# Performance work log

Measured on AMD Instinct MI355X. Metric: run time of the kernel, lower is better.

The kernel has to match this reference:

```python
import jax, jax.numpy as jnp
import numpy as np

B, F, SF = 2, 5, 15          # batch, query frames, num_shots*sframe
C, KD, VD = 1024, 128, 512   # encoder_dim, keydim, valdim
H = W = 32                   # l3 feature map (output stride 8 on 256x256)


def _conv(x, w, b, pad):
    y = jax.lax.conv_general_dilated(
        x, w, window_strides=(1, 1), padding=[(pad, pad), (pad, pad)],
        dimension_numbers=("NCHW", "OIHW", "NCHW"))
    return y + b[None, :, None, None]


def setup_inputs() -> dict:
    key = jax.random.key(0)
    ks = jax.random.split(key, 8)
    s = 0.02
    return {
        "query_feat": jax.random.normal(ks[0], (B * F, C, H, W), jnp.float32),
        "support_fg_feat": jax.random.normal(ks[1], (B * SF, C, H, W), jnp.float32),
        "w_sk": jax.random.normal(ks[2], (KD, C, 3, 3), jnp.float32) * s,
        "b_sk": jnp.zeros((KD,), jnp.float32),
        "w_sv": jax.random.normal(ks[3], (VD, C, 3, 3), jnp.float32) * s,
        "b_sv": jnp.zeros((VD,), jnp.float32),
        "w_qq": jax.random.normal(ks[4], (KD, C, 3, 3), jnp.float32) * s,
        "b_qq": jnp.zeros((KD,), jnp.float32),
        "w_qk": jax.random.normal(ks[5], (KD, C, 3, 3), jnp.float32) * s,
        "b_qk": jnp.zeros((KD,), jnp.float32),
        "w_cq": jax.random.normal(ks[6], (VD, C, 1, 1), jnp.float32) * s,
        "b_cq": jnp.zeros((VD,), jnp.float32),
    }


def reference(query_feat, support_fg_feat, w_sk, b_sk, w_sv, b_sv,
              w_qq, b_qq, w_qk, b_qk, w_cq, b_cq):
    hw = H * W
    # QKV projections (3x3 convs)
    sk = _conv(support_fg_feat, w_sk, b_sk, 1)   # [B*SF, KD, H, W]
    sv = _conv(support_fg_feat, w_sv, b_sv, 1)   # [B*SF, VD, H, W]
    qq = _conv(query_feat, w_qq, b_qq, 1)        # [B*F, KD, H, W]
    qk = _conv(query_feat, w_qk, b_qk, 1)        # [B*F, KD, H, W]

    # support K: [B, SF*hw, KD];  support V: [B, VD, SF*hw]
    support_k = sk.reshape(B, SF, KD, H, W).transpose(0, 2, 1, 3, 4)
    support_k = support_k.reshape(B, KD, SF * hw).transpose(0, 2, 1)
    support_v = sv.reshape(B, SF, VD, H, W).transpose(0, 2, 1, 3, 4)
    support_v = support_v.reshape(B, VD, SF * hw)

    qq5 = qq.reshape(B, F, KD, H, W)
    qk5 = qk.reshape(B, F, KD, H, W)
    mid = F // 2
    scale = 1.0 / jnp.sqrt(jnp.float32(KD))

    # stage 1: middle-frame query attends into support memory
    middle_q = qq5[:, mid].reshape(B, KD, hw)                 # [B, KD, hw]
    P1 = jnp.einsum("bkc,bcq->bkq", support_k, middle_q) * scale  # [B, SF*hw, hw]
    P1 = jax.nn.softmax(P1, axis=1)
    new_V = jnp.einsum("bvk,bkq->bvq", support_v, P1)          # [B, VD, hw]

    # stage 2: all-frame queries attend into middle-frame keys
    middle_K = qk5[:, mid].reshape(B, KD, hw).transpose(0, 2, 1)   # [B, hw, KD]
    qq_flat = qq5.transpose(0, 2, 1, 3, 4).reshape(B, KD, F * hw)  # [B, KD, F*hw]
    P2 = jnp.einsum("bkc,bcq->bkq", middle_K, qq_flat) * scale     # [B, hw, F*hw]
    P2 = jax.nn.softmax(P2, axis=1)
    Out = jnp.einsum("bvk,bkq->bvq", new_V, P2)                    # [B, VD, F*hw]

    after = Out.reshape(B, VD, F, H, W).transpose(0, 2, 1, 3, 4)
    after = after.reshape(B * F, VD, H, W)
    qf = _conv(query_feat, w_cq, b_cq, 0)                          # [B*F, VD, H, W]
    return jnp.concatenate([after, qf], axis=1)                    # [B*F, 2*VD, H, W]
```

## Files before the change

kernel.cpp:

```cpp
#include <hip/hip_runtime.h>
#include <cstdint>

typedef unsigned short u16;
typedef __attribute__((ext_vector_type(8))) u16 u16x8;
typedef __attribute__((ext_vector_type(4))) u16 u16x4;
typedef __attribute__((ext_vector_type(8))) _Float16 f16x8;
typedef __attribute__((ext_vector_type(4))) float f32x4;

__device__ __forceinline__ u16 f2h(float f) {
  _Float16 h = (_Float16)f;
  return __builtin_bit_cast(u16, h);
}
__device__ __forceinline__ float h2f(u16 b) {
  _Float16 h = __builtin_bit_cast(_Float16, b);
  return (float)h;
}
__device__ __forceinline__ void gll16(const void* g, void* l) {
  auto gp = reinterpret_cast<const __attribute__((address_space(1))) unsigned int*>(
      reinterpret_cast<uintptr_t>(g));
  auto lp = reinterpret_cast<__attribute__((address_space(3))) unsigned int*>(
      reinterpret_cast<uintptr_t>(l));
  __builtin_amdgcn_global_load_lds(gp, lp, 16, 0, 0);
}

__global__ __launch_bounds__(256) void pad_nhwc(const float* __restrict__ in,
                                                u16* __restrict__ outp) {
  const int img = blockIdx.x >> 5;
  const int y   = blockIdx.x & 31;
  __shared__ float tile[32][33];
  const int tid = threadIdx.x;
  u16* base = outp + (long)img * 34 * 34 * 1024;
  const u16x8 z8 = {0, 0, 0, 0, 0, 0, 0, 0};
  {
    u16* r = base + (long)(y + 1) * 34 * 1024;
    if (tid < 128) *(u16x8*)&r[tid * 8] = z8;
    else *(u16x8*)&r[33 * 1024 + (tid - 128) * 8] = z8;
  }
  if (y == 0) {
    for (int i = tid * 8; i < 34816; i += 2048) *(u16x8*)&base[i] = z8;
  }
  if (y == 31) {
    u16* r = base + 33L * 34 * 1024;
    for (int i = tid * 8; i < 34816; i += 2048) *(u16x8*)&r[i] = z8;
  }
  const int xi = tid & 31, ci = tid >> 5;
  const int xo = tid >> 3, q = tid & 7;
  const float* ip = in + (long)img * 1048576 + y * 32;
  u16* op = base + ((long)(y + 1) * 34 + 1) * 1024;
  for (int c0 = 0; c0 < 1024; c0 += 32) {
#pragma unroll
    for (int k2 = 0; k2 < 4; k2++)
      tile[k2 * 8 + ci][xi] = ip[(long)(c0 + k2 * 8 + ci) * 1024 + xi];
    __syncthreads();
    u16x4 o4;
#pragma unroll
    for (int r = 0; r < 4; r++) o4[r] = f2h(tile[q * 4 + r][xo]);
    *(u16x4*)&op[(long)xo * 1024 + c0 + q * 4] = o4;
    __syncthreads();
  }
}

__device__ __forceinline__ void wre3_body(const float* __restrict__ wp,
                                          u16* __restrict__ op, float* buf) {
  for (int i = threadIdx.x; i < 9216; i += 256) buf[i] = wp[i];
  __syncthreads();
  for (int k = threadIdx.x; k < 9216; k += 256) {
    int t = k >> 10, c = k & 1023;
    op[k] = f2h(buf[c * 9 + t]);
  }
}
__global__ __launch_bounds__(256) void wprep(
    const float* __restrict__ w_sk, const float* __restrict__ w_sv,
    const float* __restrict__ w_qq, const float* __restrict__ w_qk,
    const float* __restrict__ w_cq, u16* __restrict__ WTSK,
    u16* __restrict__ WTSV, u16* __restrict__ WTQQK, u16* __restrict__ WCQ) {
  __shared__ float buf[9216];
  const int b = blockIdx.x;
  if (b < 128) {
    wre3_body(w_sk + (long)b * 9216, WTSK + (long)b * 9216, buf);
  } else if (b < 640) {
    const int oc = b - 128;
    wre3_body(w_sv + (long)oc * 9216, WTSV + (long)oc * 9216, buf);
  } else if (b < 768) {
    const int oc = b - 640;
    wre3_body(w_qq + (long)oc * 9216, WTQQK + (long)oc * 9216, buf);
  } else if (b < 896) {
    const int oc = b - 768;
    wre3_body(w_qk + (long)oc * 9216, WTQQK + (long)(oc + 128) * 9216, buf);
  } else {
    const int i = (b - 896) * 1024 + threadIdx.x * 4;
#pragma unroll
    for (int r = 0; r < 4; r++) WCQ[i + r] = f2h(w_cq[i + r]);
  }
}

__global__ __launch_bounds__(256) void row_softmax60(u16* __restrict__ P) {
  u16* p = P + (long)blockIdx.x * 15360;
  const int tid = threadIdx.x;
  __shared__ float rm[4], rs[4];
  u16x4 v[15];
#pragma unroll
  for (int j = 0; j < 15; j++)
    v[j] = *(const u16x4*)(p + ((tid + (j << 8)) << 2));
  float m = -3.0e38f;
#pragma unroll
  for (int j = 0; j < 15; j++)
#pragma unroll
    for (int e = 0; e < 4; e++) m = fmaxf(m, h2f(v[j][e]));
#pragma unroll
  for (int o = 32; o > 0; o >>= 1) m = fmaxf(m, __shfl_xor(m, o, 64));
  if ((tid & 63) == 0) rm[tid >> 6] = m;
  __syncthreads();
  const float M = fmaxf(fmaxf(rm[0], rm[1]), fmaxf(rm[2], rm[3]));
  float s = 0.f;
#pragma unroll
  for (int j = 0; j < 15; j++)
#pragma unroll
    for (int e = 0; e < 4; e++) s += __expf(h2f(v[j][e]) - M);
#pragma unroll
  for (int o = 32; o > 0; o >>= 1) s += __shfl_xor(s, o, 64);
  if ((tid & 63) == 0) rs[tid >> 6] = s;
  __syncthreads();
  const float inv = 1.0f / (rs[0] + rs[1] + rs[2] + rs[3]);
#pragma unroll
  for (int j = 0; j < 15; j++) {
    u16x4 o4;
#pragma unroll
    for (int e = 0; e < 4; e++) o4[e] = f2h(__expf(h2f(v[j][e]) - M) * inv);
    *(u16x4*)(p + ((tid + (j << 8)) << 2)) = o4;
  }
}

__global__ __launch_bounds__(256) void row_softmax4(u16* __restrict__ P) {
  u16* p = P + (long)blockIdx.x * 1024;
  const int tid = threadIdx.x;
  __shared__ float rm[4], rs[4];
  u16x4 v = *(const u16x4*)(p + (tid << 2));
  float m = fmaxf(fmaxf(h2f(v[0]), h2f(v[1])), fmaxf(h2f(v[2]), h2f(v[3])));
#pragma unroll
  for (int o = 32; o > 0; o >>= 1) m = fmaxf(m, __shfl_xor(m, o, 64));
  if ((tid & 63) == 0) rm[tid >> 6] = m;
  __syncthreads();
  const float M = fmaxf(fmaxf(rm[0], rm[1]), fmaxf(rm[2], rm[3]));
  float s = 0.f;
#pragma unroll
  for (int e = 0; e < 4; e++) s += __expf(h2f(v[e]) - M);
#pragma unroll
  for (int o = 32; o > 0; o >>= 1) s += __shfl_xor(s, o, 64);
  if ((tid & 63) == 0) rs[tid >> 6] = s;
  __syncthreads();
  const float inv = 1.0f / (rs[0] + rs[1] + rs[2] + rs[3]);
  u16x4 o4;
#pragma unroll
  for (int e = 0; e < 4; e++) o4[e] = f2h(__expf(h2f(v[e]) - M) * inv);
  *(u16x4*)(p + (tid << 2)) = o4;
}

__global__ __launch_bounds__(256) void reduce4(const float* __restrict__ part,
                                               u16* __restrict__ o) {
  long j = ((long)blockIdx.x * 256 + threadIdx.x) * 4;
  int b = (int)(j >> 19);
  long i = j & 524287;
  const float* p = part + (long)b * 2097152 + i;
  f32x4 s = *(const f32x4*)&p[0];
#pragma unroll
  for (int c = 1; c < 4; c++) s = s + *(const f32x4*)&p[(long)c * 524288];
  u16x4 o4;
#pragma unroll
  for (int r = 0; r < 4; r++) o4[r] = f2h(s[r]);
  *(u16x4*)&o[j] = o4;
}
__global__ __launch_bounds__(256) void reduce_sk(const float* __restrict__ part,
                                                 const float* __restrict__ bias,
                                                 u16* __restrict__ o) {
  long i = ((long)blockIdx.x * 256 + threadIdx.x) * 4;
  f32x4 s = *(const f32x4*)&part[i];
  s = s + *(const f32x4*)&part[i + 3932160];
  f32x4 bb = *(const f32x4*)&bias[(int)(i & 127)];
  u16x4 o4;
#pragma unroll
  for (int r = 0; r < 4; r++) o4[r] = f2h(s[r] + bb[r]);
  *(u16x4*)&o[i] = o4;
}
__global__ __launch_bounds__(256) void reduce_qqk(
    const float* __restrict__ part, const float* __restrict__ b_qq,
    const float* __restrict__ b_qk, u16* __restrict__ QQR,
    u16* __restrict__ QKR) {
  long i = ((long)blockIdx.x * 256 + threadIdx.x) * 4;
  const int n = (int)(i >> 8), m = (int)(i & 255);
  f32x4 s = *(const f32x4*)&part[i];
  s = s + *(const f32x4*)&part[i + 2621440];
  const int lo = (m < 128);
  const int mm = m & 127;
  const float* bs = lo ? b_qq : b_qk;
  f32x4 bb = *(const f32x4*)&bs[mm];
  u16* dst = (lo ? QQR : QKR) + (long)n * 128 + mm;
  u16x4 o4;
#pragma unroll
  for (int r = 0; r < 4; r++) o4[r] = f2h(s[r] + bb[r]);
  *(u16x4*)dst = o4;
}

__global__ __launch_bounds__(512, 1)
void gemm256(const u16* __restrict__ A, const u16* __restrict__ B,
             const float* __restrict__ bias, u16* __restrict__ out) {
  __shared__ u16 lds[65536];
  const int tid = threadIdx.x, lane = tid & 63, wave = tid >> 6;
  const int nwg = gridDim.x * gridDim.y;
  int wg = blockIdx.x + gridDim.x * blockIdx.y;
  wg = (wg & 7) * (nwg >> 3) + (wg >> 3);
  const int ntile = wg % gridDim.x;
  const int mtile = wg / gridDim.x;

  const int slog = (lane & 7) ^ ((lane >> 3) & 7);
  const u16* aS[4];
  const u16* bS[4];
  int aD[4], bD[4];
#pragma unroll
  for (int j = 0; j < 4; j++) {
    const int r = wave * 32 + j * 8 + (lane >> 3);
    aS[j] = A + (long)(mtile * 256 + r) * 9216 + slog * 8;
    aD[j] = (wave * 32 + j * 8) * 64;
    const int n = ntile * 256 + r;
    const int img = n >> 10, p = n & 1023;
    const int y = p >> 5, x = p & 31;
    bS[j] = B + ((long)((img * 34 + y) * 34 + x)) * 1024 + slog * 8;
    bD[j] = 16384 + (wave * 32 + j * 8) * 64;
  }

  const int g = lane >> 4, l15 = lane & 15;
  const int wm = wave >> 2, wn = wave & 3;
  int aRow[8], bRow[4], sx[2];
#pragma unroll
  for (int mi = 0; mi < 8; mi++) aRow[mi] = (wm * 128 + mi * 16 + l15) * 64;
#pragma unroll
  for (int ni = 0; ni < 4; ni++) bRow[ni] = 16384 + (wn * 64 + ni * 16 + l15) * 64;
#pragma unroll
  for (int ks = 0; ks < 2; ks++) sx[ks] = ((ks * 4 + g) ^ (l15 & 7)) * 8;

  f32x4 acc[8][4];
  const f32x4 zero = {0.f, 0.f, 0.f, 0.f};
#pragma unroll
  for (int i = 0; i < 8; i++)
#pragma unroll
    for (int j = 0; j < 4; j++) acc[i][j] = zero;

  const int nkt = 144;
  {
#pragma unroll
    for (int j = 0; j < 4; j++) gll16(aS[j], &lds[aD[j]]);
#pragma unroll
    for (int j = 0; j < 4; j++) gll16(bS[j], &lds[bD[j]]);
    asm volatile("s_waitcnt vmcnt(0)" ::: "memory");
    __builtin_amdgcn_s_barrier();
  }

  for (int kt = 0; kt < nkt; ++kt) {
    const int buf = (kt & 1) << 15;
    const int nbuf = buf ^ 32768;
    const bool st = (kt + 1 < nkt);
    const int kb1 = (kt + 1) << 6;
    int bAdd = 0;
    if (st) {
      const int t = kb1 >> 10, c0 = kb1 & 1023;
      const int dy = t / 3, dx = t - dy * 3;
      bAdd = (dy * 34 + dx) * 1024 + c0;
    }
    f16x8 afr[4], bfr[4];
#pragma unroll
    for (int mi = 0; mi < 4; mi++) afr[mi] = *(const f16x8*)&lds[buf + aRow[mi] + sx[0]];
#pragma unroll
    for (int ni = 0; ni < 4; ni++) bfr[ni] = *(const f16x8*)&lds[buf + bRow[ni] + sx[0]];
    if (st) {
      gll16(aS[0] + kb1, &lds[nbuf + aD[0]]);
      gll16(aS[1] + kb1, &lds[nbuf + aD[1]]);
      gll16(bS[0] + bAdd, &lds[nbuf + bD[0]]);
      gll16(bS[1] + bAdd, &lds[nbuf + bD[1]]);
    }
    __builtin_amdgcn_s_barrier();
    __builtin_amdgcn_s_setprio(1);
#pragma unroll
    for (int mi = 0; mi < 4; mi++)
#pragma unroll
      for (int ni = 0; ni < 4; ni++)
        acc[mi][ni] = __builtin_amdgcn_mfma_f32_16x16x32_f16(afr[mi], bfr[ni], acc[mi][ni], 0, 0, 0);
    __builtin_amdgcn_s_setprio(0);
    __builtin_amdgcn_s_barrier();
#pragma unroll
    for (int mi = 0; mi < 4; mi++) afr[mi] = *(const f16x8*)&lds[buf + aRow[mi + 4] + sx[0]];
    if (st) {
      gll16(aS[2] + kb1, &lds[nbuf + aD[2]]);
      gll16(aS[3] + kb1, &lds[nbuf + aD[3]]);
      gll16(bS[2] + bAdd, &lds[nbuf + bD[2]]);
      gll16(bS[3] + bAdd, &lds[nbuf + bD[3]]);
    }
    __builtin_amdgcn_s_barrier();
    __builtin_amdgcn_s_setprio(1);
#pragma unroll
    for (int mi = 0; mi < 4; mi++)
#pragma unroll
      for (int ni = 0; ni < 4; ni++)
        acc[mi + 4][ni] = __builtin_amdgcn_mfma_f32_16x16x32_f16(afr[mi], bfr[ni], acc[mi + 4][ni], 0, 0, 0);
    __builtin_amdgcn_s_setprio(0);
    __builtin_amdgcn_s_barrier();
#pragma unroll
    for (int mi = 0; mi < 4; mi++) afr[mi] = *(const f16x8*)&lds[buf + aRow[mi] + sx[1]];
#pragma unroll
    for (int ni = 0; ni < 4; ni++) bfr[ni] = *(const f16x8*)&lds[buf + bRow[ni] + sx[1]];
    __builtin_amdgcn_s_barrier();
    __builtin_amdgcn_s_setprio(1);
#pragma unroll
    for (int mi = 0; mi < 4; mi++)
#pragma unroll
      for (int ni = 0; ni < 4; ni++)
        acc[mi][ni] = __builtin_amdgcn_mfma_f32_16x16x32_f16(afr[mi], bfr[ni], acc[mi][ni], 0, 0, 0);
    __builtin_amdgcn_s_setprio(0);
    __builtin_amdgcn_s_barrier();
#pragma unroll
    for (int mi = 0; mi < 4; mi++) afr[mi] = *(const f16x8*)&lds[buf + aRow[mi + 4] + sx[1]];
    __builtin_amdgcn_s_barrier();
    __builtin_amdgcn_s_setprio(1);
#pragma unroll
    for (int mi = 0; mi < 4; mi++)
#pragma unroll
      for (int ni = 0; ni < 4; ni++)
        acc[mi + 4][ni] = __builtin_amdgcn_mfma_f32_16x16x32_f16(afr[mi], bfr[ni], acc[mi + 4][ni], 0, 0, 0);
    __builtin_amdgcn_s_setprio(0);
    asm volatile("s_waitcnt vmcnt(0)" ::: "memory");
    __builtin_amdgcn_s_barrier();
  }

  const int b0 = 0;
  (void)b0;
#pragma unroll
  for (int mi = 0; mi < 8; mi++) {
#pragma unroll
    for (int ni = 0; ni < 4; ni++) {
      f32x4 v = acc[mi][ni];
      const int m0 = mtile * 256 + wm * 128 + mi * 16 + g * 4;
      const int n = ntile * 256 + wn * 64 + ni * 16 + l15;
      const int b = (n >= 15360) ? 1 : 0;
      const int rem = n - b * 15360;
#pragma unroll
      for (int r = 0; r < 4; r++) {
        const int m = m0 + r;
        out[(long)b * 7864320 + (long)m * 15360 + rem] = f2h(v[r] + bias[m]);
      }
    }
  }
}

template <int BMODE, int EPI, int SPLITK>
__global__ __launch_bounds__(256, 2)
void gemm_nt(const u16* __restrict__ A, long Azoff, int Astride,
             const u16* __restrict__ B, long Bzoff, int Bstride,
             int K, float scale,
             const float* __restrict__ bias, const float* __restrict__ bias2,
             void* __restrict__ out0, void* __restrict__ out1,
             long out_zoff, int ldo) {
  __shared__ u16 lds[4 * 8192];
  const int tid = threadIdx.x;
  const int lane = tid & 63;
  const int wave = tid >> 6;
  const int mtile = blockIdx.y, ntile = blockIdx.x, z = blockIdx.z;

  const int zb = (SPLITK > 1) ? z / SPLITK : z;
  const int zc = (SPLITK > 1) ? z % SPLITK : 0;
  const u16* Ab = A + (long)zb * Azoff + (long)zc * K;
  const u16* Bb = B + (long)zb * Bzoff + ((BMODE == 0) ? (long)zc * K : 0);

  const int r8 = lane >> 3;
  const int sphys = lane & 7;
  const u16* aSrc[4];
  const u16* bSrc[4];
  u16* aDst[4];
  u16* bDst[4];
#pragma unroll
  for (int i = 0; i < 4; i++) {
    const int row = wave * 32 + i * 8 + r8;
    const int slog = sphys ^ (row & 7);
    aSrc[i] = Ab + (long)(mtile * 128 + row) * Astride + slog * 8;
    if (BMODE == 0) {
      bSrc[i] = Bb + (long)(ntile * 128 + row) * Bstride + slog * 8;
    } else {
      const int n = ntile * 128 + row;
      const int img = n >> 10;
      const int p = n & 1023;
      const int y = p >> 5, x = p & 31;
      bSrc[i] = Bb + ((long)(img * 34 + y) * 34 + x) * 1024 + slog * 8;
    }
    aDst[i] = &lds[0] + (wave * 32 + i * 8) * 64;
    bDst[i] = &lds[0] + 8192 + (wave * 32 + i * 8) * 64;
  }

  const int g = lane >> 4, l15 = lane & 15;
  const int wm = wave >> 1, wn = wave & 1;
  int offA[2][4], offB[2][4];
#pragma unroll
  for (int ks = 0; ks < 2; ks++) {
    const int sl = ks * 4 + g;
#pragma unroll
    for (int i = 0; i < 4; i++) {
      const int ra = wm * 64 + i * 16 + l15;
      offA[ks][i] = ra * 64 + ((sl ^ (ra & 7)) * 8);
      const int rb = wn * 64 + i * 16 + l15;
      offB[ks][i] = 8192 + rb * 64 + ((sl ^ (rb & 7)) * 8);
    }
  }

  auto stage = [&](int buf, int kb) {
    int bAdd;
    if (BMODE == 0) {
      bAdd = kb;
    } else if (BMODE == 1) {
      const int kbg = zc * K + kb;
      const int t = kbg >> 10, c0 = kbg & 1023;
      const int dy = t / 3, dx = t - dy * 3;
      bAdd = (dy * 34 + dx) * 1024 + c0;
    } else {
      bAdd = 35 * 1024 + kb;
    }
    const int bufo = buf * 16384;
#pragma unroll
    for (int i = 0; i < 4; i++) gll16(aSrc[i] + kb, aDst[i] + bufo);
#pragma unroll
    for (int i = 0; i < 4; i++) gll16(bSrc[i] + bAdd, bDst[i] + bufo);
  };

  f32x4 acc[4][4];
  const f32x4 zero = {0.f, 0.f, 0.f, 0.f};
#pragma unroll
  for (int i = 0; i < 4; i++)
#pragma unroll
    for (int j = 0; j < 4; j++) acc[i][j] = zero;

  const int nkt = K >> 6;
  stage(0, 0);
  __syncthreads();
  for (int kt = 0; kt < nkt; ++kt) {
    const int buf = kt & 1;
    if (kt + 1 < nkt) stage(buf ^ 1, (kt + 1) << 6);
#pragma unroll
    for (int ks = 0; ks < 2; ks++) {
      f16x8 af[4], bfg[4];
#pragma unroll
      for (int i = 0; i < 4; i++)
        af[i] = *(const f16x8*)&lds[buf * 16384 + offA[ks][i]];
#pragma unroll
      for (int i = 0; i < 4; i++)
        bfg[i] = *(const f16x8*)&lds[buf * 16384 + offB[ks][i]];
#pragma unroll
      for (int mi = 0; mi < 4; mi++)
#pragma unroll
        for (int ni = 0; ni < 4; ni++)
          acc[mi][ni] = __builtin_amdgcn_mfma_f32_16x16x32_f16(
              af[mi], bfg[ni], acc[mi][ni], 0, 0, 0);
    }
    __syncthreads();
  }

#pragma unroll
  for (int mi = 0; mi < 4; mi++) {
#pragma unroll
    for (int ni = 0; ni < 4; ni++) {
      f32x4 v = acc[mi][ni];
      const int m0 = mtile * 128 + wm * 64 + mi * 16 + g * 4;
      const int n = ntile * 128 + wn * 64 + ni * 16 + l15;
      if (EPI == 0) {
        u16* ob = (u16*)out0;
        const float* bs = bias;
        int mm = m0;
        if (out1 != nullptr && m0 >= 128) { ob = (u16*)out1; bs = bias2; mm = m0 - 128; }
        u16x4 pk;
#pragma unroll
        for (int r = 0; r < 4; r++) {
          float val = v[r] * scale + (bs ? bs[mm + r] : 0.f);
          pk[r] = f2h(val);
        }
        *(u16x4*)&ob[(long)n * ldo + mm] = pk;
      } else if (EPI == 1) {
        u16* ob = (u16*)out0 + (long)z * out_zoff;
#pragma unroll
        for (int r = 0; r < 4; r++) {
          const int m = m0 + r;
          float val = v[r] * scale + (bias ? bias[m] : 0.f);
          ob[(long)m * ldo + n] = f2h(val);
        }
      } else if (EPI == 2) {
        float* of = (float*)out0;
        const int img = n >> 10, p = n & 1023;
#pragma unroll
        for (int r = 0; r < 4; r++) {
          const int m = m0 + r;
          of[(long)img * 1048576 + (long)(512 + m) * 1024 + p] =
              v[r] + (bias ? bias[m] : 0.f);
        }
      } else if (EPI == 3) {
        float* of = (float*)out0;
        const int f = n >> 10, p = n & 1023;
#pragma unroll
        for (int r = 0; r < 4; r++) {
          const int m = m0 + r;
          of[(long)z * 5242880 + (long)f * 1048576 + (long)m * 1024 + p] = v[r];
        }
      } else if (EPI == 4) {
        float* of = (float*)out0 + (long)z * out_zoff;
#pragma unroll
        for (int r = 0; r < 4; r++) of[(long)(m0 + r) * ldo + n] = v[r];
      } else {
        float* of = (float*)out0 + (long)zc * out_zoff;
        *(f32x4*)&of[(long)n * ldo + m0] = v;
      }
    }
  }
}

extern "C" void kernel_launch(void* const* d_in, const int* in_sizes, int n_in,
                              void* d_out, int out_size, void* d_ws, size_t ws_size,
                              hipStream_t stream) {
  (void)in_sizes; (void)n_in; (void)out_size;
  const float* query   = (const float*)d_in[0];
  const float* support = (const float*)d_in[1];
  const float* w_sk = (const float*)d_in[2];  const float* b_sk = (const float*)d_in[3];
  const float* w_sv = (const float*)d_in[4];  const float* b_sv = (const float*)d_in[5];
  const float* w_qq = (const float*)d_in[6];  const float* b_qq = (const float*)d_in[7];
  const float* w_qk = (const float*)d_in[8];  const float* b_qk = (const float*)d_in[9];
  const float* w_cq = (const float*)d_in[10]; const float* b_cq = (const float*)d_in[11];
  float* out = (float*)d_out;
  char* ws = (char*)d_ws;

  if (ws_size < 158924800u) return;

  u16* PQ    = (u16*)(ws + 0);
  u16* PS    = (u16*)(ws + 23674880);
  u16* WTSK  = (u16*)(ws + 94699520);
  u16* WTSV  = (u16*)(ws + 97058816);
  u16* WTQQK = (u16*)(ws + 106496000);
  u16* WCQ   = (u16*)(ws + 111214592);
  u16* SKR   = (u16*)(ws + 112263168);
  u16* SVA   = (u16*)(ws + 120127488);
  u16* QQR   = (u16*)(ws + 151584768);
  u16* QKR   = (u16*)(ws + 154206208);
  u16* NEWV  = (u16*)(ws + 156827648);
  u16* P1T   = PS;
  u16* P2T   = PQ;
  float* PART  = (float*)(ws + 94699520);
  float* PARTK = (float*)SVA;
  float* PARTQ = (float*)SVA;

  const float SCALE = 0.08838834764831843f;

  pad_nhwc<<<dim3(320), 256, 0, stream>>>(query, PQ);
  pad_nhwc<<<dim3(960), 256, 0, stream>>>(support, PS);
  wprep<<<dim3(1408), 256, 0, stream>>>(w_sk, w_sv, w_qq, w_qk, w_cq,
                                        WTSK, WTSV, WTQQK, WCQ);

  gemm_nt<1, 5, 2><<<dim3(240, 1, 2), 256, 0, stream>>>(
      WTSK, 0, 9216, PS, 0, 0, 4608, 1.0f, nullptr, nullptr, PARTK, nullptr,
      3932160L, 128);
  reduce_sk<<<dim3(3840), 256, 0, stream>>>(PARTK, b_sk, SKR);

  gemm_nt<1, 5, 2><<<dim3(80, 2, 2), 256, 0, stream>>>(
      WTQQK, 0, 9216, PQ, 0, 0, 4608, 1.0f, nullptr, nullptr, PARTQ, nullptr,
      2621440L, 256);
  reduce_qqk<<<dim3(2560), 256, 0, stream>>>(PARTQ, b_qq, b_qk, QQR, QKR);

  gemm256<<<dim3(120, 2), 512, 0, stream>>>(WTSV, PS, b_sv, SVA);

  gemm_nt<2, 2, 1><<<dim3(80, 4, 1), 256, 0, stream>>>(
      WCQ, 0, 1024, PQ, 0, 0, 1024, 1.0f, b_cq, nullptr, out, nullptr, 0, 0);

  gemm_nt<0, 1, 1><<<dim3(120, 8, 2), 256, 0, stream>>>(
      QQR + 262144, 655360L, 128, SKR, 1966080L, 128, 128, SCALE, nullptr,
      nullptr, P1T, nullptr, 15728640L, 15360);
  row_softmax60<<<dim3(2048), 256, 0, stream>>>(P1T);
  gemm_nt<0, 4, 4><<<dim3(8, 4, 8), 256, 0, stream>>>(
      SVA, 7864320L, 15360, P1T, 15728640L, 15360, 3840, 1.0f, nullptr,
      nullptr, PART, nullptr, 524288L, 1024);
  reduce4<<<dim3(1024), 256, 0, stream>>>(PART, NEWV);

  gemm_nt<0, 1, 1><<<dim3(8, 40, 2), 256, 0, stream>>>(
      QQR, 655360L, 128, QKR + 262144, 655360L, 128, 128, SCALE, nullptr,
      nullptr, P2T, nullptr, 5242880L, 1024);
  row_softmax4<<<dim3(10240), 256, 0, stream>>>(P2T);
  gemm_nt<0, 3, 1><<<dim3(40, 4, 2), 256, 0, stream>>>(
      NEWV, 524288L, 1024, P2T, 5242880L, 1024, 1024, 1.0f, nullptr, nullptr,
      out, nullptr, 0, 0);
}
```

Before: 696.9 us.

## Triple-buffer B tiles in conv GEMM and split-K newV GEMM into fp16 partials

```diff
diff --git a/kernel.cpp b/kernel.cpp
--- a/kernel.cpp
+++ b/kernel.cpp
@@ -156,18 +156,19 @@
   *(u16x4*)(p + (tid << 2)) = o4;
 }
 
-__global__ __launch_bounds__(256) void reduce4(const float* __restrict__ part,
-                                               u16* __restrict__ o) {
+__global__ __launch_bounds__(256) void reduce8h(const u16* __restrict__ part,
+                                                u16* __restrict__ o) {
   long j = ((long)blockIdx.x * 256 + threadIdx.x) * 4;
   int b = (int)(j >> 19);
   long i = j & 524287;
-  const float* p = part + (long)b * 2097152 + i;
-  f32x4 s = *(const f32x4*)&p[0];
-#pragma unroll
-  for (int c = 1; c < 4; c++) s = s + *(const f32x4*)&p[(long)c * 524288];
-  u16x4 o4;
-#pragma unroll
-  for (int r = 0; r < 4; r++) o4[r] = f2h(s[r]);
+  const u16* p = part + (long)b * 4194304 + i;
+  float s0 = 0.f, s1 = 0.f, s2 = 0.f, s3 = 0.f;
+#pragma unroll
+  for (int c = 0; c < 8; c++) {
+    u16x4 v = *(const u16x4*)&p[(long)c * 524288];
+    s0 += h2f(v[0]); s1 += h2f(v[1]); s2 += h2f(v[2]); s3 += h2f(v[3]);
+  }
+  u16x4 o4 = {f2h(s0), f2h(s1), f2h(s2), f2h(s3)};
   *(u16x4*)&o[j] = o4;
 }
 __global__ __launch_bounds__(256) void reduce_sk(const float* __restrict__ part,
@@ -204,7 +205,7 @@
 __global__ __launch_bounds__(512, 1)
 void gemm256(const u16* __restrict__ A, const u16* __restrict__ B,
              const float* __restrict__ bias, u16* __restrict__ out) {
-  __shared__ u16 lds[65536];
+  __shared__ u16 lds[81920];
   const int tid = threadIdx.x, lane = tid & 63, wave = tid >> 6;
   const int nwg = gridDim.x * gridDim.y;
   int wg = blockIdx.x + gridDim.x * blockIdx.y;
@@ -225,7 +226,7 @@
     const int img = n >> 10, p = n & 1023;
     const int y = p >> 5, x = p & 31;
     bS[j] = B + ((long)((img * 34 + y) * 34 + x)) * 1024 + slog * 8;
-    bD[j] = 16384 + (wave * 32 + j * 8) * 64;
+    bD[j] = (wave * 32 + j * 8) * 64;
   }
 
   const int g = lane >> 4, l15 = lane & 15;
@@ -234,9 +235,15 @@
 #pragma unroll
   for (int mi = 0; mi < 8; mi++) aRow[mi] = (wm * 128 + mi * 16 + l15) * 64;
 #pragma unroll
-  for (int ni = 0; ni < 4; ni++) bRow[ni] = 16384 + (wn * 64 + ni * 16 + l15) * 64;
+  for (int ni = 0; ni < 4; ni++) bRow[ni] = (wn * 64 + ni * 16 + l15) * 64;
 #pragma unroll
   for (int ks = 0; ks < 2; ks++) sx[ks] = ((ks * 4 + g) ^ (l15 & 7)) * 8;
+
+  auto conv_badd = [](int kb) {
+    const int t = kb >> 10, c0 = kb & 1023;
+    const int dy = t / 3, dx = t - dy * 3;
+    return (dy * 34 + dx) * 1024 + c0;
+  };
 
   f32x4 acc[8][4];
   const f32x4 zero = {0.f, 0.f, 0.f, 0.f};
@@ -249,33 +256,34 @@
   {
 #pragma unroll
     for (int j = 0; j < 4; j++) gll16(aS[j], &lds[aD[j]]);
-#pragma unroll
-    for (int j = 0; j < 4; j++) gll16(bS[j], &lds[bD[j]]);
-    asm volatile("s_waitcnt vmcnt(0)" ::: "memory");
-    __builtin_amdgcn_s_barrier();
-  }
-
+    const int b0 = conv_badd(0), b1 = conv_badd(64);
+#pragma unroll
+    for (int j = 0; j < 4; j++) gll16(bS[j] + b0, &lds[32768 + bD[j]]);
+#pragma unroll
+    for (int j = 0; j < 4; j++) gll16(bS[j] + b1, &lds[49152 + bD[j]]);
+    asm volatile("s_waitcnt vmcnt(4)" ::: "memory");
+    __builtin_amdgcn_s_barrier();
+  }
+
+  int bc = 0;
   for (int kt = 0; kt < nkt; ++kt) {
-    const int buf = (kt & 1) << 15;
-    const int nbuf = buf ^ 32768;
-    const bool st = (kt + 1 < nkt);
-    const int kb1 = (kt + 1) << 6;
-    int bAdd = 0;
-    if (st) {
-      const int t = kb1 >> 10, c0 = kb1 & 1023;
-      const int dy = t / 3, dx = t - dy * 3;
-      bAdd = (dy * 34 + dx) * 1024 + c0;
-    }
+    const int abuf = (kt & 1) << 14;
+    const int anbuf = abuf ^ 16384;
+    const int bbuf = 32768 + bc * 16384;
+    int bsn = bc + 2; if (bsn >= 3) bsn -= 3;
+    const int bnbuf = 32768 + bsn * 16384;
+    const bool stA = (kt + 1 < nkt);
+    const bool stB = (kt + 2 < nkt);
+    const int kA = (kt + 1) << 6;
+    const int bAdd2 = stB ? conv_badd((kt + 2) << 6) : 0;
     f16x8 afr[4], bfr[4];
 #pragma unroll
-    for (int mi = 0; mi < 4; mi++) afr[mi] = *(const f16x8*)&lds[buf + aRow[mi] + sx[0]];
-#pragma unroll
-    for (int ni = 0; ni < 4; ni++) bfr[ni] = *(const f16x8*)&lds[buf + bRow[ni] + sx[0]];
-    if (st) {
-      gll16(aS[0] + kb1, &lds[nbuf + aD[0]]);
-      gll16(aS[1] + kb1, &lds[nbuf + aD[1]]);
-      gll16(bS[0] + bAdd, &lds[nbuf + bD[0]]);
-      gll16(bS[1] + bAdd, &lds[nbuf + bD[1]]);
+    for (int mi = 0; mi < 4; mi++) afr[mi] = *(const f16x8*)&lds[abuf + aRow[mi] + sx[0]];
+#pragma unroll
+    for (int ni = 0; ni < 4; ni++) bfr[ni] = *(const f16x8*)&lds[bbuf + bRow[ni] + sx[0]];
+    if (stA) {
+      gll16(aS[0] + kA, &lds[anbuf + aD[0]]);
+      gll16(aS[1] + kA, &lds[anbuf + aD[1]]);
     }
     __builtin_amdgcn_s_barrier();
     __builtin_amdgcn_s_setprio(1);
@@ -287,12 +295,10 @@
     __builtin_amdgcn_s_setprio(0);
     __builtin_amdgcn_s_barrier();
 #pragma unroll
-    for (int mi = 0; mi < 4; mi++) afr[mi] = *(const f16x8*)&lds[buf + aRow[mi + 4] + sx[0]];
-    if (st) {
-      gll16(aS[2] + kb1, &lds[nbuf + aD[2]]);
-      gll16(aS[3] + kb1, &lds[nbuf + aD[3]]);
-      gll16(bS[2] + bAdd, &lds[nbuf + bD[2]]);
-      gll16(bS[3] + bAdd, &lds[nbuf + bD[3]]);
+    for (int mi = 0; mi < 4; mi++) afr[mi] = *(const f16x8*)&lds[abuf + aRow[mi + 4] + sx[0]];
+    if (stA) {
+      gll16(aS[2] + kA, &lds[anbuf + aD[2]]);
+      gll16(aS[3] + kA, &lds[anbuf + aD[3]]);
     }
     __builtin_amdgcn_s_barrier();
     __builtin_amdgcn_s_setprio(1);
@@ -304,9 +310,13 @@
     __builtin_amdgcn_s_setprio(0);
     __builtin_amdgcn_s_barrier();
 #pragma unroll
-    for (int mi = 0; mi < 4; mi++) afr[mi] = *(const f16x8*)&lds[buf + aRow[mi] + sx[1]];
-#pragma unroll
-    for (int ni = 0; ni < 4; ni++) bfr[ni] = *(const f16x8*)&lds[buf + bRow[ni] + sx[1]];
+    for (int mi = 0; mi < 4; mi++) afr[mi] = *(const f16x8*)&lds[abuf + aRow[mi] + sx[1]];
+#pragma unroll
+    for (int ni = 0; ni < 4; ni++) bfr[ni] = *(const f16x8*)&lds[bbuf + bRow[ni] + sx[1]];
+    if (stB) {
+      gll16(bS[0] + bAdd2, &lds[bnbuf + bD[0]]);
+      gll16(bS[1] + bAdd2, &lds[bnbuf + bD[1]]);
+    }
     __builtin_amdgcn_s_barrier();
     __builtin_amdgcn_s_setprio(1);
 #pragma unroll
@@ -317,7 +327,11 @@
     __builtin_amdgcn_s_setprio(0);
     __builtin_amdgcn_s_barrier();
 #pragma unroll
-    for (int mi = 0; mi < 4; mi++) afr[mi] = *(const f16x8*)&lds[buf + aRow[mi + 4] + sx[1]];
+    for (int mi = 0; mi < 4; mi++) afr[mi] = *(const f16x8*)&lds[abuf + aRow[mi + 4] + sx[1]];
+    if (stB) {
+      gll16(bS[2] + bAdd2, &lds[bnbuf + bD[2]]);
+      gll16(bS[3] + bAdd2, &lds[bnbuf + bD[3]]);
+    }
     __builtin_amdgcn_s_barrier();
     __builtin_amdgcn_s_setprio(1);
 #pragma unroll
@@ -326,12 +340,15 @@
       for (int ni = 0; ni < 4; ni++)
         acc[mi + 4][ni] = __builtin_amdgcn_mfma_f32_16x16x32_f16(afr[mi], bfr[ni], acc[mi + 4][ni], 0, 0, 0);
     __builtin_amdgcn_s_setprio(0);
-    asm volatile("s_waitcnt vmcnt(0)" ::: "memory");
-    __builtin_amdgcn_s_barrier();
-  }
-
-  const int b0 = 0;
-  (void)b0;
+    if (stB) {
+      asm volatile("s_waitcnt vmcnt(4)" ::: "memory");
+    } else if (stA) {
+      asm volatile("s_waitcnt vmcnt(0)" ::: "memory");
+    }
+    __builtin_amdgcn_s_barrier();
+    bc = bc + 1; if (bc >= 3) bc -= 3;
+  }
+
 #pragma unroll
   for (int mi = 0; mi < 8; mi++) {
 #pragma unroll
@@ -507,9 +524,13 @@
         float* of = (float*)out0 + (long)z * out_zoff;
 #pragma unroll
         for (int r = 0; r < 4; r++) of[(long)(m0 + r) * ldo + n] = v[r];
-      } else {
+      } else if (EPI == 5) {
         float* of = (float*)out0 + (long)zc * out_zoff;
         *(f32x4*)&of[(long)n * ldo + m0] = v;
+      } else {
+        u16* ob = (u16*)out0 + (long)z * out_zoff;
+#pragma unroll
+        for (int r = 0; r < 4; r++) ob[(long)(m0 + r) * ldo + n] = f2h(v[r]);
       }
     }
   }
@@ -544,7 +565,7 @@
   u16* NEWV  = (u16*)(ws + 156827648);
   u16* P1T   = PS;
   u16* P2T   = PQ;
-  float* PART  = (float*)(ws + 94699520);
+  u16* PART2 = (u16*)(ws + 94699520);
   float* PARTK = (float*)SVA;
   float* PARTQ = (float*)SVA;
 
@@ -574,10 +595,10 @@
       QQR + 262144, 655360L, 128, SKR, 1966080L, 128, 128, SCALE, nullptr,
       nullptr, P1T, nullptr, 15728640L, 15360);
   row_softmax60<<<dim3(2048), 256, 0, stream>>>(P1T);
-  gemm_nt<0, 4, 4><<<dim3(8, 4, 8), 256, 0, stream>>>(
-      SVA, 7864320L, 15360, P1T, 15728640L, 15360, 3840, 1.0f, nullptr,
-      nullptr, PART, nullptr, 524288L, 1024);
-  reduce4<<<dim3(1024), 256, 0, stream>>>(PART, NEWV);
+  gemm_nt<0, 6, 8><<<dim3(8, 4, 16), 256, 0, stream>>>(
+      SVA, 7864320L, 15360, P1T, 15728640L, 15360, 1920, 1.0f, nullptr,
+      nullptr, PART2, nullptr, 524288L, 1024);
+  reduce8h<<<dim3(1024), 256, 0, stream>>>(PART2, NEWV);
 
   gemm_nt<0, 1, 1><<<dim3(8, 40, 2), 256, 0, stream>>>(
       QQR, 655360L, 128, QKR + 262144, 655360L, 128, 128, SCALE, nullptr,
```

Measured after the change: 686.5 us. About the same (-1.5%).
